# Optimization experiments

Measured on AMD Instinct MI355X. Metric: run time of the kernel, lower is better.

## Reference

```python
import jax, jax.numpy as jnp
import numpy as np

C_NUM, D_NUM = 64, 128
N_NODES = C_NUM * D_NUM + C_NUM + D_NUM  # 8384
HEADS, OUT = 4, 256


def gat_conv(h, src, dst, W, al, ar, b):
    """DGL-style GATConv (eval mode, attn_drop off). h:[N,F], W:[F,H*O], al/ar:[H,O], b:[H*O]."""
    N = h.shape[0]
    H, O = al.shape
    feat = (h @ W).reshape(N, H, O)
    el = jnp.sum(feat * al, axis=-1)                      # [N,H]
    er = jnp.sum(feat * ar, axis=-1)
    e = jax.nn.leaky_relu(el[src] + er[dst], 0.2)         # [E,H]
    m = jax.ops.segment_max(e, dst, num_segments=N)
    m = jnp.where(jnp.isfinite(m), m, 0.0)
    p = jnp.exp(e - m[dst])
    s = jax.ops.segment_sum(p, dst, num_segments=N)
    a = p / jnp.maximum(s[dst], 1e-9)                     # edge softmax per dst, per head
    out = jax.ops.segment_sum(a[:, :, None] * feat[src], dst, num_segments=N)  # [N,H,O]
    return out + b.reshape(1, H, O)


def cagat_layer(edges, dfeat, cvec, gw, al, ar, gb,
                wq_w, wq_b, wk_w, wk_b, wv_w, wv_b, ip_w, ip_b, op_w, op_b):
    ch = cvec.shape[1]
    pad = jnp.repeat(cvec, D_NUM, axis=0)                       # [c*d, ch]
    pad3 = jnp.broadcast_to(cvec.mean(axis=0), (D_NUM, ch))      # [d, ch]
    cfin = jnp.concatenate([pad, cvec, pad3], axis=0)            # [N, ch]
    inf = jnp.concatenate([dfeat, cfin], axis=1)                 # [N, F+ch]
    # 4 relation-specific GATConvs, stacked (HeteroGraphConv aggregate='stack')
    rst = jnp.stack([gat_conv(inf, edges[t, 0], edges[t, 1], gw[t], al[t], ar[t], gb[t])
                     for t in range(4)], axis=1)                 # [N,4,H,O]
    N = inf.shape[0]
    rst = rst.reshape(N, 4 * HEADS, OUT)
    E = OUT
    Q = (cfin @ wq_w + wq_b)[:, None, :]                         # [N,1,E]
    K = rst @ wk_w + wk_b                                        # [N,16,E]
    V = rst @ wv_w + wv_b
    # nn.MultiheadAttention(E, 1): in-proj then single-head SDPA then out-proj
    q = Q @ ip_w[:E].T + ip_b[:E]
    k = K @ ip_w[E:2 * E].T + ip_b[E:2 * E]
    v = V @ ip_w[2 * E:].T + ip_b[2 * E:]
    att = jax.nn.softmax(jnp.einsum('nqe,nke->nqk', q, k) / jnp.sqrt(jnp.float32(E)), axis=-1)
    o = jnp.einsum('nqk,nke->nqe', att, v) @ op_w.T + op_b
    return o.reshape(N, E)


def setup_inputs() -> dict:
    key = jax.random.key(0)
    ks = iter(jax.random.split(key, 64))
    rn = lambda shape: jax.random.normal(next(ks), shape, jnp.float32) * 0.05
    inp = {}
    inp['x'] = rn((D_NUM, 256))
    inp['cf'] = rn((C_NUM, 512))
    inp['cf_net_w'] = rn((512, 128)); inp['cf_net_b'] = rn((128,))
    inp['ht_w'] = rn((512, 256)); inp['ht_b'] = rn((256,))
    for l in ('1', '2'):
        inp['gw' + l] = rn((4, 384, HEADS * OUT))
        inp['al' + l] = rn((4, HEADS, OUT))
        inp['ar' + l] = rn((4, HEADS, OUT))
        inp['gb' + l] = rn((4, HEADS * OUT))
        inp['wq' + l + '_w'] = rn((128, 256)); inp['wq' + l + '_b'] = rn((256,))
        inp['wk' + l + '_w'] = rn((256, 256)); inp['wk' + l + '_b'] = rn((256,))
        inp['wv' + l + '_w'] = rn((256, 256)); inp['wv' + l + '_b'] = rn((256,))
        inp['ip' + l + '_w'] = rn((768, 256)); inp['ip' + l + '_b'] = rn((768,))
        inp['op' + l + '_w'] = rn((256, 256)); inp['op' + l + '_b'] = rn((256,))
    inp['edges'] = jax.random.randint(next(ks), (4, 2, 50000), 0, N_NODES, dtype=jnp.int32)
    return inp


def reference(x, cf, cf_net_w, cf_net_b, ht_w, ht_b,
              gw1, al1, ar1, gb1, wq1_w, wq1_b, wk1_w, wk1_b, wv1_w, wv1_b, ip1_w, ip1_b, op1_w, op1_b,
              gw2, al2, ar2, gb2, wq2_w, wq2_b, wk2_w, wk2_b, wv2_w, wv2_b, ip2_w, ip2_b, op2_w, op2_b,
              edges):
    cf_vec = cf @ cf_net_w + cf_net_b                           # [c, cell_hidden]
    d_pad = jnp.tile(x, (C_NUM, 1))                             # [c*d, in]
    d_uc = cf @ ht_w + ht_b                                     # [c, in]
    d_feat = jnp.concatenate([d_pad, d_uc, x], axis=0)          # [N, in]
    h = cagat_layer(edges, d_feat, cf_vec, gw1, al1, ar1, gb1,
                    wq1_w, wq1_b, wk1_w, wk1_b, wv1_w, wv1_b, ip1_w, ip1_b, op1_w, op1_b)
    h = cagat_layer(edges, h, cf_vec, gw2, al2, ar2, gb2,
                    wq2_w, wq2_b, wk2_w, wk2_b, wv2_w, wv2_b, ip2_w, ip2_b, op2_w, op2_b)
    return h
```

## Files before the change

### kernel.cpp

```cpp
#include <hip/hip_runtime.h>
#include <hip/hip_bf16.h>

typedef __hip_bfloat16 bf16;
typedef __attribute__((ext_vector_type(8))) short short8;
typedef __attribute__((ext_vector_type(4))) short short4v;
typedef __attribute__((ext_vector_type(4))) float f32x4;

#define KN 8384
#define KNPAD 8448
#define KE 50000
#define NBIG 4480

__device__ __forceinline__ float toF(float v){ return v; }
__device__ __forceinline__ float toF(bf16 v){ return __bfloat162float(v); }
__device__ __forceinline__ float b2f(short u){ return __uint_as_float(((unsigned int)(unsigned short)u) << 16); }
__device__ __forceinline__ void stor(float* p, float v){ *p = v; }
__device__ __forceinline__ void stor(bf16* p, float v){ *p = __float2bfloat16(v); }

__device__ __forceinline__ void glds16(const bf16* g, bf16* l){
  __builtin_amdgcn_global_load_lds(
      (const __attribute__((address_space(1))) unsigned int*)(g),
      (__attribute__((address_space(3))) unsigned int*)(l), 16, 0, 0);
}

template<typename TC>
__global__ __launch_bounds__(256)
void gemm_mfma_bt(const bf16* __restrict__ A, const bf16* __restrict__ BT,
                  const float* __restrict__ bias, TC* __restrict__ C,
                  int M, int N, int K, int ldc)
{
  __shared__ bf16 As[128 * 32];
  __shared__ bf16 Bs[128 * 32];
  const int bm = blockIdx.y * 128, bn = blockIdx.x * 128;
  const int tid = threadIdx.x;
  const int w = tid >> 6, l = tid & 63;
  const int wr = (w >> 1) * 64, wc = (w & 1) * 64;
  const int lr = l & 15;
  int rS[2], lqS[2];
  #pragma unroll
  for (int i = 0; i < 2; i++){
    rS[i] = w * 32 + i * 16 + (l >> 2);
    lqS[i] = (l & 3) ^ ((rS[i] >> 1) & 3);
  }
  const bf16* gA0 = A  + (size_t)(bm + rS[0]) * K + lqS[0] * 8;
  const bf16* gA1 = A  + (size_t)(bm + rS[1]) * K + lqS[1] * 8;
  const bf16* gB0 = BT + (size_t)(bn + rS[0]) * K + lqS[0] * 8;
  const bf16* gB1 = BT + (size_t)(bn + rS[1]) * K + lqS[1] * 8;
  bf16* lA0 = &As[w * 1024];
  bf16* lA1 = &As[w * 1024 + 512];
  bf16* lB0 = &Bs[w * 1024];
  bf16* lB1 = &Bs[w * 1024 + 512];
  f32x4 acc[4][4] = {};
  for (int k0 = 0; k0 < K; k0 += 32) {
    glds16(gA0 + k0, lA0);
    glds16(gA1 + k0, lA1);
    glds16(gB0 + k0, lB0);
    glds16(gB1 + k0, lB1);
    __syncthreads();
    short8 a[4], b[4];
    #pragma unroll
    for (int i = 0; i < 4; i++){
      int R = wr + i * 16 + lr;
      int pq = (l >> 4) ^ ((R >> 1) & 3);
      a[i] = *(short8*)&As[R * 32 + pq * 8];
    }
    #pragma unroll
    for (int j = 0; j < 4; j++){
      int R = wc + j * 16 + lr;
      int pq = (l >> 4) ^ ((R >> 1) & 3);
      b[j] = *(short8*)&Bs[R * 32 + pq * 8];
    }
    #pragma unroll
    for (int i = 0; i < 4; i++)
      #pragma unroll
      for (int j = 0; j < 4; j++)
        acc[i][j] = __builtin_amdgcn_mfma_f32_16x16x32_bf16(a[i], b[j], acc[i][j], 0, 0, 0);
    __syncthreads();
  }
  const int orow = (l >> 4) * 4, ocol = l & 15;
  #pragma unroll
  for (int i = 0; i < 4; i++){
    #pragma unroll
    for (int j = 0; j < 4; j++){
      int gcol = bn + wc + j * 16 + ocol;
      float bv = bias ? bias[gcol] : 0.f;
      #pragma unroll
      for (int rg = 0; rg < 4; rg++){
        int grow = bm + wr + i * 16 + orow + rg;
        if (grow < M) stor(&C[(size_t)grow * ldc + gcol], acc[i][j][rg] + bv);
      }
    }
  }
}

__global__ void k_transGW(const float* __restrict__ gw, bf16* __restrict__ bigBT){
  __shared__ float t[32][33];
  int rel = blockIdx.z;
  const float* B = gw + (size_t)rel * 384 * 1024;
  bf16* BT = bigBT + (size_t)rel * 1024 * 384;
  int n0 = blockIdx.x * 32, k0 = blockIdx.y * 32;
  int tx = threadIdx.x, ty = threadIdx.y;
  for (int i = ty; i < 32; i += 8)
    t[i][tx] = B[(size_t)(k0 + i) * 1024 + n0 + tx];
  __syncthreads();
  for (int i = ty; i < 32; i += 8)
    BT[(size_t)(n0 + i) * 384 + k0 + tx] = __float2bfloat16(t[tx][i]);
}

__global__ __launch_bounds__(256)
void k_galr(const float* __restrict__ gw, const float* __restrict__ al,
            const float* __restrict__ ar, bf16* __restrict__ bigBT){
  int r = blockIdx.y;
  int k = blockIdx.x * 4 + (threadIdx.x >> 6);
  int lane = threadIdx.x & 63;
  int rr = r & 15, t = rr >> 2, h = rr & 3;
  const float* wsrc = ((r < 16) ? al : ar) + t * 1024 + h * 256;
  const float* gp = gw + (size_t)t * 384 * 1024 + (size_t)k * 1024 + h * 256;
  float v = 0.f;
  #pragma unroll
  for (int i = 0; i < 4; i++){
    int o = lane + i * 64;
    v += gp[o] * wsrc[o];
  }
  #pragma unroll
  for (int off = 32; off; off >>= 1) v += __shfl_down(v, off);
  if (lane == 0) bigBT[(size_t)(4352 + r) * 384 + k] = __float2bfloat16(v);
}

__global__ void k_zpad(bf16* bigBT){
  int i = blockIdx.x * blockDim.x + threadIdx.x;
  if (i < 96 * 384) bigBT[(size_t)4384 * 384 + i] = __float2bfloat16(0.f);
}

__global__ void k_wprep(const float* __restrict__ ipw, const float* __restrict__ wkw,
                        const float* __restrict__ opw, const float* __restrict__ wvw,
                        float* __restrict__ ipwQT, float* __restrict__ wkwT,
                        float* __restrict__ opwT, float* __restrict__ wvwT){
  __shared__ float t[32][33];
  const float* S; float* D;
  switch (blockIdx.z){
    case 0: S = ipw; D = ipwQT; break;
    case 1: S = wkw; D = wkwT; break;
    case 2: S = opw; D = opwT; break;
    default: S = wvw; D = wvwT; break;
  }
  int c0 = blockIdx.x * 32, r0 = blockIdx.y * 32;
  int tx = threadIdx.x, ty = threadIdx.y;
  for (int i = ty; i < 32; i += 8)
    t[i][tx] = S[(size_t)(r0 + i) * 256 + c0 + tx];
  __syncthreads();
  for (int i = ty; i < 32; i += 8)
    D[(size_t)(c0 + i) * 256 + r0 + tx] = t[tx][i];
}

__global__ __launch_bounds__(256)
void k_fold1(const float* __restrict__ wqw, const float* __restrict__ wqb,
             const float* __restrict__ ipw, const float* __restrict__ ipb,
             const float* __restrict__ ipwQT, const float* __restrict__ wkwT,
             const float* __restrict__ opwT,
             float* __restrict__ Wq, float* __restrict__ B2,
             float* __restrict__ M1, float* __restrict__ bq){
  int b = blockIdx.x, tid = threadIdx.x;
  if (b < 128){
    int c = b; float s = 0.f;
    for (int e = 0; e < 256; e++) s += wqw[c * 256 + e] * ipwQT[e * 256 + tid];
    Wq[c * 256 + tid] = s;
  } else if (b < 384){
    int j = b - 128; float s = 0.f;
    for (int e = 0; e < 256; e++) s += wkwT[e * 256 + tid] * ipw[(256 + j) * 256 + e];
    B2[j * 256 + tid] = s;
  } else if (b < 640){
    int e = b - 384; float s = 0.f;
    for (int f = 0; f < 256; f++) s += ipw[(512 + f) * 256 + e] * opwT[f * 256 + tid];
    M1[e * 256 + tid] = s;
  } else {
    float s = 0.f;
    for (int e = 0; e < 256; e++) s += wqb[e] * ipwQT[e * 256 + tid];
    bq[tid] = s + ipb[tid];
  }
}

__global__ __launch_bounds__(256)
void k_fold2(const float* __restrict__ Wq, const float* __restrict__ B2,
             const float* __restrict__ M1, const float* __restrict__ bq,
             const float* __restrict__ wvb, const float* __restrict__ ipb,
             const float* __restrict__ opb,
             const float* __restrict__ wvwT, const float* __restrict__ opwT,
             bf16* __restrict__ bigBT, bf16* __restrict__ WvT,
             float* __restrict__ bv, float* __restrict__ biasc){
  int b = blockIdx.x, tid = threadIdx.x;
  if (b < 256){
    int d = b; float s = 0.f;
    for (int j = 0; j < 256; j++) s += Wq[d * 256 + j] * B2[j * 256 + tid];
    bigBT[(size_t)(4096 + tid) * 384 + 256 + d] = __float2bfloat16(s);
  } else if (b < 512){
    int j = b - 256; float s = 0.f;
    for (int e = 0; e < 256; e++) s += wvwT[e * 256 + tid] * M1[e * 256 + j];
    WvT[j * 256 + tid] = __float2bfloat16(s);
  } else {
    float b2 = 0.f;
    for (int j = 0; j < 256; j++) b2 += bq[j] * B2[j * 256 + tid];
    float s = 0.f;
    for (int e = 0; e < 256; e++) s += wvb[e] * M1[e * 256 + tid];
    for (int f = 0; f < 256; f++) s += ipb[512 + f] * opwT[f * 256 + tid];
    bv[tid] = s + opb[tid];
    for (int i = tid; i < NBIG; i += 256)
      biasc[i] = (i - 4096 == tid) ? b2 : 0.f;
    for (int k = 0; k < 256; k++)
      bigBT[(size_t)(4096 + tid) * 384 + k] = __float2bfloat16(0.f);
  }
}

__global__ __launch_bounds__(384)
void k_pre(const float* __restrict__ cf, const float* __restrict__ cfw, const float* __restrict__ cfb,
           const float* __restrict__ htw, const float* __restrict__ htb,
           float* __restrict__ cfvec, float* __restrict__ duc)
{
  int c = blockIdx.x;
  int col = threadIdx.x;
  __shared__ float row[512];
  for (int i = col; i < 512; i += 384) row[i] = cf[c * 512 + i];
  __syncthreads();
  if (col < 128){
    float acc = cfb[col];
    for (int k = 0; k < 512; k++) acc += row[k] * cfw[k * 128 + col];
    cfvec[c * 128 + col] = acc;
  } else {
    int j = col - 128;
    float acc = htb[j];
    for (int k = 0; k < 512; k++) acc += row[k] * htw[k * 256 + j];
    duc[c * 256 + j] = acc;
  }
}
__global__ void k_mean(const float* cv, float* m){
  int o = threadIdx.x;
  float s = 0.f;
  for (int c = 0; c < 64; c++) s += cv[c * 128 + o];
  m[o] = s * (1.f / 64.f);
}
__global__ void k_dfeatinf(const float* x, const float* duc, bf16* inf){
  int n = blockIdx.x, o = threadIdx.x;
  float v;
  if (n < 8192)      v = x[(n & 127) * 256 + o];
  else if (n < 8256) v = duc[(n - 8192) * 256 + o];
  else               v = x[(n - 8256) * 256 + o];
  inf[(size_t)n * 384 + o] = __float2bfloat16(v);
}
__global__ void k_cfininf(const float* cv, const float* cm, bf16* inf){
  int n = blockIdx.x, o = threadIdx.x;
  float v;
  if (n < 8192)      v = cv[(n >> 7) * 128 + o];
  else if (n < 8256) v = cv[(n - 8192) * 128 + o];
  else               v = cm[o];
  inf[(size_t)n * 384 + 256 + o] = __float2bfloat16(v);
}
__global__ void k_zeroi(int* p, int n){
  int i = blockIdx.x * blockDim.x + threadIdx.x; if (i < n) p[i] = 0;
}
__global__ void k_copyi(const int* a, int* b, int n){
  int i = blockIdx.x * blockDim.x + threadIdx.x; if (i < n) b[i] = a[i];
}
__global__ void k_countB(const int* __restrict__ edges, int* __restrict__ cnt){
  int i = blockIdx.x * blockDim.x + threadIdx.x;
  if (i < 4 * KE){
    int t = i / KE, idx = i - t * KE;
    int d = edges[t * 2 * KE + KE + idx];
    atomicAdd(&cnt[t * KN + d], 1);
  }
}
__global__ void k_fillB(const int* __restrict__ edges, int* __restrict__ cur, int* __restrict__ csrc){
  int i = blockIdx.x * blockDim.x + threadIdx.x;
  if (i < 4 * KE){
    int t = i / KE, idx = i - t * KE;
    int s = edges[t * 2 * KE + idx];
    int d = edges[t * 2 * KE + KE + idx];
    int p = atomicAdd(&cur[t * KN + d], 1);
    csrc[p] = s;
  }
}
__global__ void k_scan(const int* __restrict__ cnt, int* __restrict__ ptr, int n){
  __shared__ int part[1024];
  int tid = threadIdx.x;
  const int CH = (n + 1023) >> 10;
  int base = tid * CH;
  int s = 0;
  for (int i = 0; i < CH; i++){ int idx = base + i; if (idx < n) s += cnt[idx]; }
  part[tid] = s; __syncthreads();
  for (int off = 1; off < 1024; off <<= 1){
    int v = (tid >= off) ? part[tid - off] : 0;
    __syncthreads();
    part[tid] += v;
    __syncthreads();
  }
  int run = part[tid] - s;
  for (int i = 0; i < CH; i++){
    int idx = base + i;
    if (idx < n){ ptr[idx] = run; run += cnt[idx]; }
  }
  if (tid == 1023) ptr[n] = part[1023];
}

__global__ __launch_bounds__(256)
void k_aggattn(const int* __restrict__ ptr, const int* __restrict__ csrc,
               const bf16* __restrict__ big, const float* __restrict__ gb,
               bf16* __restrict__ rbar)
{
  const int n = blockIdx.x, tid = threadIdx.x;
  const int h4 = tid & 3, j0 = tid >> 2;
  const int w = tid >> 6, lane = tid & 63;
  const int head = w, c4 = lane * 4;
  __shared__ float s_rst[16][260];
  __shared__ float s_sc[16];
  __shared__ float sinv4[4];
  __shared__ float partial[16];
  __shared__ float sa[64][4];
  __shared__ int ssrc[64];
  for (int t = 0; t < 4; t++){
    const int beg = ptr[t * KN + n], deg = ptr[t * KN + n + 1] - beg;
    const int elc = 4352 + t * 4 + h4;
    float ern = toF(big[(size_t)n * NBIG + 4368 + t * 4 + h4]);
    float sum = 0.f;
    for (int j = j0; j < deg; j += 64){
      int s = csrc[beg + j];
      float e = toF(big[(size_t)s * NBIG + elc]) + ern;
      e = e > 0.f ? e : 0.2f * e;
      sum += __expf(e);
    }
    #pragma unroll
    for (int off = 4; off < 64; off <<= 1) sum += __shfl_xor(sum, off);
    if (lane < 4) partial[w * 4 + lane] = sum;
    __syncthreads();
    if (tid < 4){
      float s0 = partial[tid] + partial[4 + tid] + partial[8 + tid] + partial[12 + tid];
      sinv4[tid] = 1.f / fmaxf(s0, 1e-9f);
    }
    __syncthreads();
    float acc0 = 0.f, acc1 = 0.f, acc2 = 0.f, acc3 = 0.f;
    const size_t foff = (size_t)t * 1024 + head * 256 + c4;
    for (int c0 = 0; c0 < deg; c0 += 64){
      int cn = min(64, deg - c0);
      if (tid < cn) ssrc[tid] = csrc[beg + c0 + tid];
      __syncthreads();
      if (j0 < cn){
        int s = ssrc[j0];
        float e = toF(big[(size_t)s * NBIG + elc]) + ern;
        e = e > 0.f ? e : 0.2f * e;
        sa[j0][h4] = __expf(e) * sinv4[h4];
      }
      __syncthreads();
      for (int j = 0; j < cn; j++){
        int s = ssrc[j];
        float wj = sa[j][head];
        short4v v = *(const short4v*)&big[(size_t)s * NBIG + foff];
        acc0 += wj * b2f(v[0]);
        acc1 += wj * b2f(v[1]);
        acc2 += wj * b2f(v[2]);
        acc3 += wj * b2f(v[3]);
      }
      __syncthreads();
    }
    const float* gbh = gb + t * 1024 + head * 256 + c4;
    float* rp = &s_rst[t * 4 + head][c4];
    rp[0] = acc0 + gbh[0];
    rp[1] = acc1 + gbh[1];
    rp[2] = acc2 + gbh[2];
    rp[3] = acc3 + gbh[3];
    __syncthreads();
  }
  const bf16* q = big + (size_t)n * NBIG + 4096;
  #pragma unroll
  for (int si = 0; si < 4; si++){
    int s = w * 4 + si;
    float v = 0.f;
    #pragma unroll
    for (int i = 0; i < 4; i++){
      int o = lane + i * 64;
      v += s_rst[s][o] * toF(q[o]);
    }
    #pragma unroll
    for (int off = 32; off; off >>= 1) v += __shfl_down(v, off);
    if (lane == 0) s_sc[s] = v * 0.0625f;
  }
  __syncthreads();
  float sc[16]; float m = -1e30f;
  #pragma unroll
  for (int s = 0; s < 16; s++){ sc[s] = s_sc[s]; m = fmaxf(m, sc[s]); }
  float sum = 0.f;
  #pragma unroll
  for (int s = 0; s < 16; s++){ sc[s] = __expf(sc[s] - m); sum += sc[s]; }
  float inv = 1.f / sum;
  float r = 0.f;
  #pragma unroll
  for (int s = 0; s < 16; s++) r += sc[s] * s_rst[s][tid];
  rbar[(size_t)n * 256 + tid] = __float2bfloat16(r * inv);
}

struct LWT {
  const float *gw, *al, *ar, *gb, *wqw, *wqb, *wkw, *wkb, *wvw, *wvb, *ipw, *ipb, *opw, *opb;
};

extern "C" void kernel_launch(void* const* d_in, const int* in_sizes, int n_in,
                              void* d_out, int out_size, void* d_ws, size_t ws_size,
                              hipStream_t stream)
{
  const float* x   = (const float*)d_in[0];
  const float* cf  = (const float*)d_in[1];
  const float* cfw = (const float*)d_in[2];
  const float* cfb = (const float*)d_in[3];
  const float* htw = (const float*)d_in[4];
  const float* htb = (const float*)d_in[5];
  LWT L[2];
  for (int l = 0; l < 2; l++){
    int b = 6 + l * 14;
    L[l].gw  = (const float*)d_in[b + 0];
    L[l].al  = (const float*)d_in[b + 1];
    L[l].ar  = (const float*)d_in[b + 2];
    L[l].gb  = (const float*)d_in[b + 3];
    L[l].wqw = (const float*)d_in[b + 4];
    L[l].wqb = (const float*)d_in[b + 5];
    L[l].wkw = (const float*)d_in[b + 6];
    L[l].wkb = (const float*)d_in[b + 7];
    L[l].wvw = (const float*)d_in[b + 8];
    L[l].wvb = (const float*)d_in[b + 9];
    L[l].ipw = (const float*)d_in[b + 10];
    L[l].ipb = (const float*)d_in[b + 11];
    L[l].opw = (const float*)d_in[b + 12];
    L[l].opb = (const float*)d_in[b + 13];
  }
  const int* edges = (const int*)d_in[34];

  char* w = (char*)d_ws;
  size_t off = 0;
  auto alc = [&](size_t bytes) -> void* {
    off = (off + 255) & ~(size_t)255;
    void* p = w + off; off += bytes; return p;
  };
  float* f_cfvec = (float*)alc(64 * 128 * 4);
  float* f_cfmean= (float*)alc(128 * 4);
  float* f_duc   = (float*)alc(64 * 256 * 4);
  bf16*  b_inf   = (bf16*) alc((size_t)KNPAD * 384 * 2);
  bf16*  b_big   = (bf16*) alc((size_t)KN * NBIG * 2);
  bf16*  b_bigBT = (bf16*) alc((size_t)NBIG * 384 * 2);
  float* f_biasc = (float*)alc((size_t)NBIG * 4);
  bf16*  b_rbar  = (bf16*) alc((size_t)KNPAD * 256 * 2);
  float* f_Wq    = (float*)alc(128 * 256 * 4);
  float* f_B2    = (float*)alc(256 * 256 * 4);
  float* f_M1    = (float*)alc(256 * 256 * 4);
  float* f_bq    = (float*)alc(256 * 4);
  float* f_bv    = (float*)alc(256 * 4);
  bf16*  b_WvT   = (bf16*) alc(256 * 256 * 2);
  float* f_ipwQT = (float*)alc(256 * 256 * 4);
  float* f_wkwT  = (float*)alc(256 * 256 * 4);
  float* f_opwT  = (float*)alc(256 * 256 * 4);
  float* f_wvwT  = (float*)alc(256 * 256 * 4);
  int*   i_ptr   = (int*)  alc((size_t)(4 * KN + 1) * 4);
  int*   i_src   = (int*)  alc((size_t)4 * KE * 4);
  int*   i_cnt   = (int*)  alc((size_t)4 * KN * 4);
  int*   i_cur   = (int*)  alc((size_t)4 * KN * 4);
  if (off > ws_size) return;

  k_pre<<<64, 384, 0, stream>>>(cf, cfw, cfb, htw, htb, f_cfvec, f_duc);
  k_mean<<<1, 128, 0, stream>>>(f_cfvec, f_cfmean);
  k_dfeatinf<<<KN, 256, 0, stream>>>(x, f_duc, b_inf);
  k_cfininf <<<KN, 128, 0, stream>>>(f_cfvec, f_cfmean, b_inf);
  k_zpad<<<(96 * 384 + 255) / 256, 256, 0, stream>>>(b_bigBT);

  k_zeroi<<<(4 * KN + 255) / 256, 256, 0, stream>>>(i_cnt, 4 * KN);
  k_countB<<<(4 * KE + 255) / 256, 256, 0, stream>>>(edges, i_cnt);
  k_scan<<<1, 1024, 0, stream>>>(i_cnt, i_ptr, 4 * KN);
  k_copyi<<<(4 * KN + 255) / 256, 256, 0, stream>>>(i_ptr, i_cur, 4 * KN);
  k_fillB<<<(4 * KE + 255) / 256, 256, 0, stream>>>(edges, i_cur, i_src);

  auto run_layer = [&](const LWT& Wt, bool last){
    k_transGW<<<dim3(32, 12, 4), dim3(32, 8), 0, stream>>>(Wt.gw, b_bigBT);
    k_galr<<<dim3(96, 32), 256, 0, stream>>>(Wt.gw, Wt.al, Wt.ar, b_bigBT);
    k_wprep<<<dim3(8, 8, 4), dim3(32, 8), 0, stream>>>(Wt.ipw, Wt.wkw, Wt.opw, Wt.wvw,
                                                       f_ipwQT, f_wkwT, f_opwT, f_wvwT);
    k_fold1<<<641, 256, 0, stream>>>(Wt.wqw, Wt.wqb, Wt.ipw, Wt.ipb,
                                     f_ipwQT, f_wkwT, f_opwT,
                                     f_Wq, f_B2, f_M1, f_bq);
    k_fold2<<<513, 256, 0, stream>>>(f_Wq, f_B2, f_M1, f_bq, Wt.wvb, Wt.ipb, Wt.opb,
                                     f_wvwT, f_opwT,
                                     b_bigBT, b_WvT, f_bv, f_biasc);
    gemm_mfma_bt<bf16><<<dim3(NBIG / 128, 66), 256, 0, stream>>>(
        b_inf, b_bigBT, f_biasc, b_big, KN, NBIG, 384, NBIG);
    k_aggattn<<<KN, 256, 0, stream>>>(i_ptr, i_src, b_big, Wt.gb, b_rbar);
    if (last)
      gemm_mfma_bt<float><<<dim3(2, 66), 256, 0, stream>>>(
          b_rbar, b_WvT, f_bv, (float*)d_out, KN, 256, 256, 256);
    else
      gemm_mfma_bt<bf16><<<dim3(2, 66), 256, 0, stream>>>(
          b_rbar, b_WvT, f_bv, b_inf, KN, 256, 256, 384);
  };

  run_layer(L[0], false);
  run_layer(L[1], true);
}
```

Measured before the change: 582.9 us.

## Process relations per wavefront in GAT aggregation and fuse input assembly kernels

```diff
diff --git a/kernel.cpp b/kernel.cpp
--- a/kernel.cpp
+++ b/kernel.cpp
@@ -238,21 +238,23 @@
   for (int c = 0; c < 64; c++) s += cv[c * 128 + o];
   m[o] = s * (1.f / 64.f);
 }
-__global__ void k_dfeatinf(const float* x, const float* duc, bf16* inf){
+__global__ __launch_bounds__(384)
+void k_infasm(const float* __restrict__ x, const float* __restrict__ duc,
+              const float* __restrict__ cv, const float* __restrict__ cm,
+              bf16* __restrict__ inf){
   int n = blockIdx.x, o = threadIdx.x;
   float v;
-  if (n < 8192)      v = x[(n & 127) * 256 + o];
-  else if (n < 8256) v = duc[(n - 8192) * 256 + o];
-  else               v = x[(n - 8256) * 256 + o];
+  if (o < 256){
+    if (n < 8192)      v = x[(n & 127) * 256 + o];
+    else if (n < 8256) v = duc[(n - 8192) * 256 + o];
+    else               v = x[(n - 8256) * 256 + o];
+  } else {
+    int oo = o - 256;
+    if (n < 8192)      v = cv[(n >> 7) * 128 + oo];
+    else if (n < 8256) v = cv[(n - 8192) * 128 + oo];
+    else               v = cm[oo];
+  }
   inf[(size_t)n * 384 + o] = __float2bfloat16(v);
-}
-__global__ void k_cfininf(const float* cv, const float* cm, bf16* inf){
-  int n = blockIdx.x, o = threadIdx.x;
-  float v;
-  if (n < 8192)      v = cv[(n >> 7) * 128 + o];
-  else if (n < 8256) v = cv[(n - 8192) * 128 + o];
-  else               v = cm[o];
-  inf[(size_t)n * 384 + 256 + o] = __float2bfloat16(v);
 }
 __global__ void k_zeroi(int* p, int n){
   int i = blockIdx.x * blockDim.x + threadIdx.x; if (i < n) p[i] = 0;
@@ -306,67 +308,71 @@
                bf16* __restrict__ rbar)
 {
   const int n = blockIdx.x, tid = threadIdx.x;
-  const int h4 = tid & 3, j0 = tid >> 2;
   const int w = tid >> 6, lane = tid & 63;
-  const int head = w, c4 = lane * 4;
+  const int t = w;
+  const int head = lane >> 4;
   __shared__ float s_rst[16][260];
   __shared__ float s_sc[16];
-  __shared__ float sinv4[4];
-  __shared__ float partial[16];
-  __shared__ float sa[64][4];
-  __shared__ int ssrc[64];
-  for (int t = 0; t < 4; t++){
-    const int beg = ptr[t * KN + n], deg = ptr[t * KN + n + 1] - beg;
-    const int elc = 4352 + t * 4 + h4;
-    float ern = toF(big[(size_t)n * NBIG + 4368 + t * 4 + h4]);
-    float sum = 0.f;
-    for (int j = j0; j < deg; j += 64){
-      int s = csrc[beg + j];
-      float e = toF(big[(size_t)s * NBIG + elc]) + ern;
+  __shared__ float sa4[4][64][4];
+  __shared__ int ssrcW[4][64];
+  const int beg = ptr[t * KN + n], deg = ptr[t * KN + n + 1] - beg;
+  short4v e4 = *(const short4v*)&big[(size_t)n * NBIG + 4368 + t * 4];
+  float ern[4] = {b2f(e4[0]), b2f(e4[1]), b2f(e4[2]), b2f(e4[3])};
+  float sums[4] = {0.f, 0.f, 0.f, 0.f};
+  for (int j = lane; j < deg; j += 64){
+    int s = csrc[beg + j];
+    short4v l4 = *(const short4v*)&big[(size_t)s * NBIG + 4352 + t * 4];
+    #pragma unroll
+    for (int h = 0; h < 4; h++){
+      float e = b2f(l4[h]) + ern[h];
       e = e > 0.f ? e : 0.2f * e;
-      sum += __expf(e);
-    }
-    #pragma unroll
-    for (int off = 4; off < 64; off <<= 1) sum += __shfl_xor(sum, off);
-    if (lane < 4) partial[w * 4 + lane] = sum;
-    __syncthreads();
-    if (tid < 4){
-      float s0 = partial[tid] + partial[4 + tid] + partial[8 + tid] + partial[12 + tid];
-      sinv4[tid] = 1.f / fmaxf(s0, 1e-9f);
-    }
-    __syncthreads();
-    float acc0 = 0.f, acc1 = 0.f, acc2 = 0.f, acc3 = 0.f;
-    const size_t foff = (size_t)t * 1024 + head * 256 + c4;
-    for (int c0 = 0; c0 < deg; c0 += 64){
-      int cn = min(64, deg - c0);
-      if (tid < cn) ssrc[tid] = csrc[beg + c0 + tid];
-      __syncthreads();
-      if (j0 < cn){
-        int s = ssrc[j0];
-        float e = toF(big[(size_t)s * NBIG + elc]) + ern;
+      sums[h] += __expf(e);
+    }
+  }
+  #pragma unroll
+  for (int off = 32; off; off >>= 1){
+    #pragma unroll
+    for (int h = 0; h < 4; h++) sums[h] += __shfl_xor(sums[h], off);
+  }
+  float sinv[4];
+  #pragma unroll
+  for (int h = 0; h < 4; h++) sinv[h] = 1.f / fmaxf(sums[h], 1e-9f);
+  float acc[16];
+  #pragma unroll
+  for (int i = 0; i < 16; i++) acc[i] = 0.f;
+  const size_t cbase = (size_t)t * 1024 + lane * 16;
+  for (int c0 = 0; c0 < deg; c0 += 64){
+    int cn = min(64, deg - c0);
+    if (lane < cn){
+      int s = csrc[beg + c0 + lane];
+      ssrcW[t][lane] = s;
+      short4v l4 = *(const short4v*)&big[(size_t)s * NBIG + 4352 + t * 4];
+      #pragma unroll
+      for (int h = 0; h < 4; h++){
+        float e = b2f(l4[h]) + ern[h];
         e = e > 0.f ? e : 0.2f * e;
-        sa[j0][h4] = __expf(e) * sinv4[h4];
+        sa4[t][lane][h] = __expf(e) * sinv[h];
       }
-      __syncthreads();
-      for (int j = 0; j < cn; j++){
-        int s = ssrc[j];
-        float wj = sa[j][head];
-        short4v v = *(const short4v*)&big[(size_t)s * NBIG + foff];
-        acc0 += wj * b2f(v[0]);
-        acc1 += wj * b2f(v[1]);
-        acc2 += wj * b2f(v[2]);
-        acc3 += wj * b2f(v[3]);
-      }
-      __syncthreads();
-    }
-    const float* gbh = gb + t * 1024 + head * 256 + c4;
-    float* rp = &s_rst[t * 4 + head][c4];
-    rp[0] = acc0 + gbh[0];
-    rp[1] = acc1 + gbh[1];
-    rp[2] = acc2 + gbh[2];
-    rp[3] = acc3 + gbh[3];
-    __syncthreads();
-  }
+    }
+    for (int j = 0; j < cn; j++){
+      int s = ssrcW[t][j];
+      float wj = sa4[t][j][head];
+      const bf16* fp = &big[(size_t)s * NBIG + cbase];
+      short8 v0 = *(const short8*)fp;
+      short8 v1 = *(const short8*)(fp + 8);
+      #pragma unroll
+      for (int i = 0; i < 8; i++) acc[i] += wj * b2f(v0[i]);
+      #pragma unroll
+      for (int i = 0; i < 8; i++) acc[8 + i] += wj * b2f(v1[i]);
+    }
+  }
+  {
+    const float* gbp = gb + t * 1024 + lane * 16;
+    float* rp = &s_rst[t * 4 + head][(lane & 15) * 16];
+    #pragma unroll
+    for (int i = 0; i < 16; i++) rp[i] = acc[i] + gbp[i];
+  }
+  __syncthreads();
   const bf16* q = big + (size_t)n * NBIG + 4096;
   #pragma unroll
   for (int si = 0; si < 4; si++){
@@ -461,8 +467,7 @@
 
   k_pre<<<64, 384, 0, stream>>>(cf, cfw, cfb, htw, htb, f_cfvec, f_duc);
   k_mean<<<1, 128, 0, stream>>>(f_cfvec, f_cfmean);
-  k_dfeatinf<<<KN, 256, 0, stream>>>(x, f_duc, b_inf);
-  k_cfininf <<<KN, 128, 0, stream>>>(f_cfvec, f_cfmean, b_inf);
+  k_infasm<<<KN, 384, 0, stream>>>(x, f_duc, f_cfvec, f_cfmean, b_inf);
   k_zpad<<<(96 * 384 + 255) / 256, 256, 0, stream>>>(b_bigBT);
 
   k_zeroi<<<(4 * KN + 255) / 256, 256, 0, stream>>>(i_cnt, 4 * KN);
```

After: 558.5 us. 1.04x faster.
